# Performance work log

Hardware: AMD Instinct MI355X
Metric: run time of the kernel (lower is better)

The kernel has to match this reference:

```python
import jax, jax.numpy as jnp
import numpy as np

HEAD_SIZE = 64


def setup_inputs() -> dict:
    key = jax.random.key(0)
    k1, k2, k3, k4 = jax.random.split(key, 4)
    B, T, C, H = 8, 2048, 1024, HEAD_SIZE
    return {
        "idx": jax.random.normal(k1, (B, T, C), dtype=jnp.float32),
        "Wk": jax.random.normal(k2, (C, H), dtype=jnp.float32) * (C ** -0.5),
        "Wq": jax.random.normal(k3, (C, H), dtype=jnp.float32) * (C ** -0.5),
        "Wv": jax.random.normal(k4, (C, H), dtype=jnp.float32) * (C ** -0.5),
    }


def reference(idx, Wk, Wq, Wv):
    # idx: [B, T, C]; Wk/Wq/Wv: [C, H]
    B, T, C = idx.shape
    H = Wk.shape[1]
    k = idx @ Wk  # [B, T, H]
    q = idx @ Wq  # [B, T, H]
    v = idx @ Wv  # [B, T, H]
    # Faithful to source: wei = k @ q^T (note: k first, as written in the torch code)
    wei = jnp.einsum("bth,bsh->bts", k, q) * (H ** -0.5)  # [B, T, T]
    causal = jnp.tril(jnp.ones((T, T), dtype=bool))
    wei = jnp.where(causal, wei, -jnp.inf)
    wei = jax.nn.softmax(wei, axis=-1)
    # Dropout(0.5) treated as eval-mode identity (deterministic reference)
    out = jnp.einsum("bts,bsh->bth", wei, v)  # [B, T, H]
    return out
```

## Files before the change

### kernel.cpp

```cpp
#include <hip/hip_runtime.h>

#define B_ 8
#define T_ 2048
#define C_ 1024
#define H_ 64
#define BT_ (B_ * T_)

typedef float f32x4 __attribute__((ext_vector_type(4)));
typedef unsigned short u16x4 __attribute__((ext_vector_type(4)));
typedef unsigned short u16x8 __attribute__((ext_vector_type(8)));
typedef __bf16 bf16x8 __attribute__((ext_vector_type(8)));

static __device__ __forceinline__ unsigned short f2bf(float f) {
    unsigned int u = __builtin_bit_cast(unsigned int, f);
    u = (u + 0x7FFFu + ((u >> 16) & 1u)) >> 16;
    return (unsigned short)u;
}

static __device__ __forceinline__ f32x4 mfma16(u16x8 a, u16x8 b, f32x4 c) {
    return __builtin_amdgcn_mfma_f32_16x16x32_bf16(
        __builtin_bit_cast(bf16x8, a), __builtin_bit_cast(bf16x8, b), c, 0, 0, 0);
}

static __device__ __forceinline__ void cvtpk4(float a0, float a1, float a2, float a3,
                                              unsigned& d0, unsigned& d1) {
    asm("v_cvt_pk_bf16_f32 %0, %1, %2" : "=v"(d0) : "v"(a0), "v"(a1));
    asm("v_cvt_pk_bf16_f32 %0, %1, %2" : "=v"(d1) : "v"(a2), "v"(a3));
}

static __device__ __forceinline__ f32x4 bf4f(u16x4 v) {
    f32x4 r;
    r[0] = __builtin_bit_cast(float, (unsigned)v[0] << 16);
    r[1] = __builtin_bit_cast(float, (unsigned)v[1] << 16);
    r[2] = __builtin_bit_cast(float, (unsigned)v[2] << 16);
    r[3] = __builtin_bit_cast(float, (unsigned)v[3] << 16);
    return r;
}

static __device__ __forceinline__ void gload_lds16(const void* g, void* l) {
    auto gp = (const __attribute__((address_space(1))) char*)(
        reinterpret_cast<uintptr_t>(g));
    auto lp = (__attribute__((address_space(3))) char*)(
        reinterpret_cast<uintptr_t>(l));
    __builtin_amdgcn_global_load_lds(gp, lp, 16, 0, 0);
}

static __device__ __forceinline__ int Pof(int j) {
    return 5 - (j >= 2 ? 1 : 0) - (j >= 6 ? 1 : 0);
}
static __device__ __forceinline__ int offsof(int j) {
    return (j < 2) ? 5 * j : (j < 6 ? 4 * j + 2 : 3 * j + 8);
}

__global__ __launch_bounds__(256) void wprep(const float* __restrict__ Wk,
                                             const float* __restrict__ Wq,
                                             const float* __restrict__ Wv,
                                             unsigned short* __restrict__ wt) {
    __shared__ float tile[64][65];
    const int arr = blockIdx.x >> 4, ct = blockIdx.x & 15;
    const float* W = (arr == 0) ? Wk : ((arr == 1) ? Wq : Wv);
    const int tid = threadIdx.x;
    {
        int c = tid >> 2, seg = (tid & 3) << 4;
        const float* src = W + (size_t)(ct * 64 + c) * 64 + seg;
#pragma unroll
        for (int j = 0; j < 16; j += 4) {
            f32x4 v4 = *(const f32x4*)(src + j);
            tile[c][seg + j + 0] = v4[0];
            tile[c][seg + j + 1] = v4[1];
            tile[c][seg + j + 2] = v4[2];
            tile[c][seg + j + 3] = v4[3];
        }
    }
    __syncthreads();
    {
        int h = tid >> 2, cs = (tid & 3) << 4;
        unsigned short* dst = wt + (size_t)(arr * 64 + h) * 1024 + ct * 64 + cs;
#pragma unroll
        for (int j = 0; j < 16; ++j) dst[j] = f2bf(tile[cs + j][h]);
    }
}

__global__ __launch_bounds__(512, 2) void proj_gemm(const float* __restrict__ idx,
                                                    const unsigned short* __restrict__ wt,
                                                    unsigned short* __restrict__ kw,
                                                    unsigned short* __restrict__ qw,
                                                    unsigned short* __restrict__ vtw) {
    __shared__ unsigned short As[2][64 * 64];
    __shared__ unsigned short Bs[2][192 * 64];
    const int tid = threadIdx.x;
    const int lane = tid & 63, w = tid >> 6;
    const int g = lane >> 4, l15 = lane & 15;
    const int m0 = blockIdx.x * 64;
    const int ar = tid >> 3, as_ = tid & 7;

    f32x4 acc[2][3] = {};
    f32x4 areg[2][2];

    auto sloadA = [&](int set, int k0) {
        const f32x4* src = (const f32x4*)(idx + (size_t)(m0 + ar) * 1024 + k0 +
                                          ((as_ ^ (ar & 7)) * 8));
        areg[set][0] = src[0];
        areg[set][1] = src[1];
    };
    auto swriteA = [&](int set, int buf) {
        unsigned d0, d1, d2, d3;
        cvtpk4(areg[set][0][0], areg[set][0][1], areg[set][0][2], areg[set][0][3], d0, d1);
        cvtpk4(areg[set][1][0], areg[set][1][1], areg[set][1][2], areg[set][1][3], d2, d3);
        uint4 pk; pk.x = d0; pk.y = d1; pk.z = d2; pk.w = d3;
        *(uint4*)&As[buf][ar * 64 + as_ * 8] = pk;
    };
    auto stageB = [&](int k0, int buf) {
#pragma unroll
        for (int i = 0; i < 3; ++i) {
            int slot0 = i * 512 + w * 64;
            int n = i * 64 + w * 8 + (lane >> 3);
            int us = (lane & 7) ^ (lane >> 3);
            gload_lds16(wt + (size_t)n * 1024 + k0 + us * 8,
                        &Bs[buf][slot0 * 8]);
        }
    };

    stageB(0, 0);
    sloadA(0, 0);
    sloadA(1, 64);
    swriteA(0, 0);
    __syncthreads();

    for (int kt = 0; kt < 16; ++kt) {
        const int cur = kt & 1;
        if (kt < 15) stageB((kt + 1) * 64, cur ^ 1);
        if (kt < 14) sloadA(cur, (kt + 2) * 64);
#pragma unroll
        for (int ks = 0; ks < 2; ++ks) {
            u16x8 a0 = *(const u16x8*)&As[cur][((w & 1) * 16 + l15) * 64 +
                                               (((ks * 4 + g) ^ (l15 & 7)) * 8)];
            u16x8 a1 = *(const u16x8*)&As[cur][(32 + (w & 1) * 16 + l15) * 64 +
                                               (((ks * 4 + g) ^ (l15 & 7)) * 8)];
#pragma unroll
            for (int nf = 0; nf < 3; ++nf) {
                int n = (w >> 1) * 48 + nf * 16 + l15;
                u16x8 b = *(const u16x8*)&Bs[cur][n * 64 + (((ks * 4 + g) ^ (n & 7)) * 8)];
                acc[0][nf] = mfma16(a0, b, acc[0][nf]);
                acc[1][nf] = mfma16(a1, b, acc[1][nf]);
            }
        }
        if (kt < 15) swriteA(cur ^ 1, cur ^ 1);
        __syncthreads();
    }

#pragma unroll
    for (int nf = 0; nf < 3; ++nf) {
        int nb = (w >> 1) * 3 + nf;
        int arr = nb >> 2;
        int nloc = ((nb & 3) << 4) + l15;
#pragma unroll
        for (int mi = 0; mi < 2; ++mi) {
            f32x4 ac = acc[mi][nf];
            int row = m0 + mi * 32 + (w & 1) * 16 + g * 4;
            if (arr == 2) {
                u16x4 pk = {f2bf(ac[0]), f2bf(ac[1]), f2bf(ac[2]), f2bf(ac[3])};
                *(u16x4*)&vtw[(size_t)nloc * BT_ + row] = pk;
            } else {
                unsigned short* dst = arr ? qw : kw;
                dst[(size_t)(row + 0) * 64 + nloc] = f2bf(ac[0]);
                dst[(size_t)(row + 1) * 64 + nloc] = f2bf(ac[1]);
                dst[(size_t)(row + 2) * 64 + nloc] = f2bf(ac[2]);
                dst[(size_t)(row + 3) * 64 + nloc] = f2bf(ac[3]);
            }
        }
    }
}

__global__ __launch_bounds__(512, 2) void attn_part(const unsigned short* __restrict__ kw,
                                                    const unsigned short* __restrict__ qw,
                                                    const unsigned short* __restrict__ vtw,
                                                    unsigned short* __restrict__ Opart,
                                                    float* __restrict__ lpart) {
    __shared__ unsigned short q_s[2][64 * 64];
    __shared__ unsigned short v_s[2][64 * 64];
    __shared__ unsigned short p_s[8 * 32 * 64];
    const int tid = threadIdx.x;
    const int w = tid >> 6, lane = tid & 63;
    const int g = lane >> 4, l15 = lane & 15;
    const int bid = blockIdx.x;
    const int b = bid & 7;
    const int rem = bid >> 3;
    const int j = (rem < 10) ? (rem / 5) : (rem < 26 ? (rem - 2) >> 2 : (rem - 8) / 3);
    const int P = Pof(j);
    const int part = rem - offsof(j);
    const size_t base = (size_t)b * T_;
    const int tA0 = 128 * j + 16 * w;
    const int tB0 = 128 * (15 - j) + 16 * w;
    const int nS = 2 * (16 - j);
    unsigned short* p_my = p_s + w * 2048;
    const float SCL = 0.125f * 1.44269504f;
    const float MOFF = 16.0f;

    u16x8 kf[2][2];
#pragma unroll
    for (int tf = 0; tf < 2; ++tf) {
        const unsigned short* kr = kw + (size_t)(base + (tf ? tB0 : tA0) + l15) * 64;
        kf[tf][0] = *(const u16x8*)(kr + g * 8);
        kf[tf][1] = *(const u16x8*)(kr + 32 + g * 8);
    }

    f32x4 o[4][2] = {};
    float l_lane[2] = {0.f, 0.f};

    auto stageQV = [&](int st, int buf) {
        int s0 = st << 6;
        int r = w * 8 + (lane >> 3);
        int us = (lane & 7) ^ (lane >> 3);
        gload_lds16(qw + (size_t)(base + s0 + r) * 64 + us * 8,
                    &q_s[buf][w * 512]);
        gload_lds16(vtw + (size_t)r * BT_ + base + s0 + us * 8,
                    &v_s[buf][w * 512]);
    };

    stageQV(part, 0);
    __syncthreads();

    int i = 0;
    for (int st = part; st < nS; st += P, ++i) {
        const int s0 = st << 6;
        const int buf = i & 1;
        const bool more = (st + P < nS);
        if (more) stageQV(st + P, buf ^ 1);
        const bool dA = (s0 <= tA0 + 15);
        const bool dB = (s0 <= tB0 + 15);

        u16x8 a[2][4];
#pragma unroll
        for (int ks = 0; ks < 2; ++ks)
#pragma unroll
            for (int sf = 0; sf < 4; ++sf)
                a[ks][sf] = *(const u16x8*)&q_s[buf][(sf * 16 + l15) * 64 +
                                                     (((ks * 4 + g) ^ (l15 & 7)) * 8)];

        f32x4 s_[4][2] = {};
        __builtin_amdgcn_s_setprio(1);
        if (dB) {
#pragma unroll
            for (int ks = 0; ks < 2; ++ks)
#pragma unroll
                for (int sf = 0; sf < 4; ++sf)
                    s_[sf][1] = mfma16(a[ks][sf], kf[1][ks], s_[sf][1]);
        }
        if (dA) {
#pragma unroll
            for (int ks = 0; ks < 2; ++ks)
#pragma unroll
                for (int sf = 0; sf < 4; ++sf)
                    s_[sf][0] = mfma16(a[ks][sf], kf[0][ks], s_[sf][0]);
        }
        __builtin_amdgcn_s_setprio(0);

#pragma unroll
        for (int tf_ = 1; tf_ >= 0; --tf_) {
            if (tf_ ? !dB : !dA) continue;
            const int tbase_ = tf_ ? tB0 : tA0;
            float pv[4][4];
#pragma unroll
            for (int sf = 0; sf < 4; ++sf)
#pragma unroll
                for (int r = 0; r < 4; ++r)
                    pv[sf][r] = exp2f(fmaf(s_[sf][tf_][r], SCL, -MOFF));
            if (s0 + 63 > tbase_) {
                const int t_ = tbase_ + l15;
#pragma unroll
                for (int sf = 0; sf < 4; ++sf)
#pragma unroll
                    for (int r = 0; r < 4; ++r) {
                        int sg = s0 + sf * 16 + g * 4 + r;
                        if (sg > t_) pv[sf][r] = 0.f;
                    }
            }
            float lacc = 0.f;
#pragma unroll
            for (int sf = 0; sf < 4; ++sf)
                lacc += (pv[sf][0] + pv[sf][1]) + (pv[sf][2] + pv[sf][3]);
            l_lane[tf_] += lacc;
            const int trow = tf_ * 16 + l15;
#pragma unroll
            for (int sf = 0; sf < 4; ++sf) {
                unsigned r0, r1;
                cvtpk4(pv[sf][0], pv[sf][1], pv[sf][2], pv[sf][3], r0, r1);
                int u16i = (sf * 2 + (g >> 1)) ^ (l15 & 7);
                uint2 pk; pk.x = r0; pk.y = r1;
                *(uint2*)&p_my[trow * 64 + u16i * 8 + (g & 1) * 4] = pk;
            }
        }

        u16x8 vf[2][4];
#pragma unroll
        for (int ks = 0; ks < 2; ++ks)
#pragma unroll
            for (int mf = 0; mf < 4; ++mf)
                vf[ks][mf] = *(const u16x8*)&v_s[buf][(mf * 16 + l15) * 64 +
                                                      (((ks * 4 + g) ^ (l15 & 7)) * 8)];
        __builtin_amdgcn_s_setprio(1);
#pragma unroll
        for (int ks = 0; ks < 2; ++ks) {
            if (dB) {
                u16x8 bp1 = *(const u16x8*)&p_my[(16 + l15) * 64 +
                                                 (((ks * 4 + g) ^ (l15 & 7)) * 8)];
#pragma unroll
                for (int mf = 0; mf < 4; ++mf)
                    o[mf][1] = mfma16(vf[ks][mf], bp1, o[mf][1]);
            }
            if (dA) {
                u16x8 bp0 = *(const u16x8*)&p_my[l15 * 64 +
                                                 (((ks * 4 + g) ^ (l15 & 7)) * 8)];
#pragma unroll
                for (int mf = 0; mf < 4; ++mf)
                    o[mf][0] = mfma16(vf[ks][mf], bp0, o[mf][0]);
            }
        }
        __builtin_amdgcn_s_setprio(0);

        __syncthreads();
    }

#pragma unroll
    for (int tf = 0; tf < 2; ++tf) {
        float ls = l_lane[tf];
        ls += __shfl_xor(ls, 16);
        ls += __shfl_xor(ls, 32);
        int rl = tf * 128 + w * 16 + l15;
        if (g == 0) lpart[(size_t)bid * 256 + rl] = ls;
#pragma unroll
        for (int mf = 0; mf < 4; ++mf) {
            unsigned r0, r1;
            cvtpk4(o[mf][tf][0], o[mf][tf][1], o[mf][tf][2], o[mf][tf][3], r0, r1);
            uint2 pk; pk.x = r0; pk.y = r1;
            *(uint2*)&Opart[(size_t)bid * 16384 + (size_t)rl * 64 + mf * 16 + g * 4] = pk;
        }
    }
}

__global__ __launch_bounds__(256) void attn_comb(const unsigned short* __restrict__ Opart,
                                                 const float* __restrict__ lpart,
                                                 float* __restrict__ out) {
    int gt = blockIdx.x * 256 + threadIdx.x;
    int row = gt >> 4;
    int h0 = (gt & 15) << 2;
    int b = row >> 11, t = row & 2047;
    int ti = t >> 7, rit = t & 127;
    int j = (ti < 8) ? ti : (15 - ti);
    int tf = (ti < 8) ? 0 : 1;
    int rl = tf * 128 + rit;
    int P = Pof(j), offs = offsof(j);
    f32x4 acc = {};
    float L = 0.f;
    for (int p = 0; p < P; ++p) {
        int pb = b + 8 * (offs + p);
        u16x4 ov = *(const u16x4*)&Opart[(size_t)pb * 16384 + (size_t)rl * 64 + h0];
        acc += bf4f(ov);
        L += lpart[(size_t)pb * 256 + rl];
    }
    float inv = 1.f / L;
    *(f32x4*)&out[(size_t)row * 64 + h0] = acc * inv;
}

extern "C" void kernel_launch(void* const* d_in, const int* in_sizes, int n_in,
                              void* d_out, int out_size, void* d_ws, size_t ws_size,
                              hipStream_t stream) {
    const float* idx = (const float*)d_in[0];
    const float* Wk = (const float*)d_in[1];
    const float* Wq = (const float*)d_in[2];
    const float* Wv = (const float*)d_in[3];
    float* out = (float*)d_out;

    unsigned short* wt = (unsigned short*)d_ws;
    unsigned short* kw = wt + 192 * 1024;
    unsigned short* qw = kw + (size_t)BT_ * 64;
    unsigned short* vtw = qw + (size_t)BT_ * 64;
    unsigned short* Opart = (unsigned short*)((char*)d_ws + (8u << 20));
    float* lpart = (float*)((char*)d_ws + (18u << 20));

    wprep<<<48, 256, 0, stream>>>(Wk, Wq, Wv, wt);
    proj_gemm<<<256, 512, 0, stream>>>(idx, wt, kw, qw, vtw);
    attn_part<<<256, 512, 0, stream>>>(kw, qw, vtw, Opart, lpart);
    attn_comb<<<1024, 256, 0, stream>>>(Opart, lpart, out);
}
```

Before: 47.82 us.

## Fuse split-KV combine into attention kernel via last-block atomic counter

Removes the separate combine kernel launch: each attention block bumps a per-(batch, tile) atomic counter after writing its partial output, and the last finisher sums the partials and writes the normalized output. Counters are zeroed in the weight-prep kernel. This saves a launch and the gap between kernels, but the combine now runs serialized on the last block of each group, with 512 threads each handling 32 elements, which may lengthen the tail.

New measurement: 106.6 us. 123% more time.

```diff
diff --git a/kernel.cpp b/kernel.cpp
--- a/kernel.cpp
+++ b/kernel.cpp
@@ -55,7 +55,9 @@
 __global__ __launch_bounds__(256) void wprep(const float* __restrict__ Wk,
                                              const float* __restrict__ Wq,
                                              const float* __restrict__ Wv,
-                                             unsigned short* __restrict__ wt) {
+                                             unsigned short* __restrict__ wt,
+                                             int* __restrict__ cnt) {
+    if (blockIdx.x == 0 && threadIdx.x < 64) cnt[threadIdx.x] = 0;
     __shared__ float tile[64][65];
     const int arr = blockIdx.x >> 4, ct = blockIdx.x & 15;
     const float* W = (arr == 0) ? Wk : ((arr == 1) ? Wq : Wv);
@@ -176,10 +178,13 @@
                                                     const unsigned short* __restrict__ qw,
                                                     const unsigned short* __restrict__ vtw,
                                                     unsigned short* __restrict__ Opart,
-                                                    float* __restrict__ lpart) {
+                                                    float* __restrict__ lpart,
+                                                    float* __restrict__ out,
+                                                    int* __restrict__ cnt) {
     __shared__ unsigned short q_s[2][64 * 64];
     __shared__ unsigned short v_s[2][64 * 64];
     __shared__ unsigned short p_s[8 * 32 * 64];
+    __shared__ int lastf;
     const int tid = threadIdx.x;
     const int w = tid >> 6, lane = tid & 63;
     const int g = lane >> 4, l15 = lane & 15;
@@ -337,30 +342,35 @@
             *(uint2*)&Opart[(size_t)bid * 16384 + (size_t)rl * 64 + mf * 16 + g * 4] = pk;
         }
     }
-}
-
-__global__ __launch_bounds__(256) void attn_comb(const unsigned short* __restrict__ Opart,
-                                                 const float* __restrict__ lpart,
-                                                 float* __restrict__ out) {
-    int gt = blockIdx.x * 256 + threadIdx.x;
-    int row = gt >> 4;
-    int h0 = (gt & 15) << 2;
-    int b = row >> 11, t = row & 2047;
-    int ti = t >> 7, rit = t & 127;
-    int j = (ti < 8) ? ti : (15 - ti);
-    int tf = (ti < 8) ? 0 : 1;
-    int rl = tf * 128 + rit;
-    int P = Pof(j), offs = offsof(j);
-    f32x4 acc = {};
-    float L = 0.f;
-    for (int p = 0; p < P; ++p) {
-        int pb = b + 8 * (offs + p);
-        u16x4 ov = *(const u16x4*)&Opart[(size_t)pb * 16384 + (size_t)rl * 64 + h0];
-        acc += bf4f(ov);
-        L += lpart[(size_t)pb * 256 + rl];
-    }
-    float inv = 1.f / L;
-    *(f32x4*)&out[(size_t)row * 64 + h0] = acc * inv;
+
+    __threadfence();
+    if (tid == 0)
+        lastf = (atomicAdd(&cnt[b * 8 + j], 1) == P - 1);
+    __syncthreads();
+    if (!lastf) return;
+
+    {
+        const int offs = offsof(j);
+        int rl = tid >> 1;
+        int h0 = (tid & 1) * 32;
+        int tf = rl >> 7, rloc = rl & 127;
+        int trow = tf ? (128 * (15 - j) + rloc) : (128 * j + rloc);
+        f32x4 acc[8] = {};
+        float L = 0.f;
+        for (int p = 0; p < P; ++p) {
+            int pb = b + 8 * (offs + p);
+            const unsigned short* src = Opart + (size_t)pb * 16384 + (size_t)rl * 64 + h0;
+            L += lpart[(size_t)pb * 256 + rl];
+#pragma unroll
+            for (int q = 0; q < 8; ++q)
+                acc[q] += bf4f(*(const u16x4*)(src + q * 4));
+        }
+        float inv = 1.f / L;
+        float* orow = out + (base + trow) * 64 + h0;
+#pragma unroll
+        for (int q = 0; q < 8; ++q)
+            *(f32x4*)(orow + q * 4) = acc[q] * inv;
+    }
 }
 
 extern "C" void kernel_launch(void* const* d_in, const int* in_sizes, int n_in,
@@ -378,9 +388,9 @@
     unsigned short* vtw = qw + (size_t)BT_ * 64;
     unsigned short* Opart = (unsigned short*)((char*)d_ws + (8u << 20));
     float* lpart = (float*)((char*)d_ws + (18u << 20));
-
-    wprep<<<48, 256, 0, stream>>>(Wk, Wq, Wv, wt);
+    int* cnt = (int*)((char*)d_ws + (20u << 20));
+
+    wprep<<<48, 256, 0, stream>>>(Wk, Wq, Wv, wt, cnt);
     proj_gemm<<<256, 512, 0, stream>>>(idx, wt, kw, qw, vtw);
-    attn_part<<<256, 512, 0, stream>>>(kw, qw, vtw, Opart, lpart);
-    attn_comb<<<1024, 256, 0, stream>>>(Opart, lpart, out);
-}
+    attn_part<<<256, 512, 0, stream>>>(kw, qw, vtw, Opart, lpart, out, cnt);
+}
```
